# Kernel tuning notes

Measured on AMD Instinct MI355X. Metric: run time of the kernel, lower is better.

Reference implementation:

```python
import jax, jax.numpy as jnp
import numpy as np

SEQ, B, IN, H, L = 256, 512, 300, 512, 256
EPS = 1e-5


def setup_inputs() -> dict:
    key = jax.random.key(0)
    ks = jax.random.split(key, 10)
    s_ih = 1.0 / np.sqrt(H)
    return {
        "x": jax.random.normal(ks[0], (SEQ, B, IN), dtype=jnp.float32),
        "W_ih": jax.random.normal(ks[1], (4 * H, IN), dtype=jnp.float32) * s_ih,
        "W_hh": jax.random.normal(ks[2], (4 * H, H), dtype=jnp.float32) * s_ih,
        "b_ih": jax.random.normal(ks[3], (4 * H,), dtype=jnp.float32) * s_ih,
        "b_hh": jax.random.normal(ks[4], (4 * H,), dtype=jnp.float32) * s_ih,
        "bn1_gamma": jnp.ones((H,), dtype=jnp.float32),
        "bn1_beta": jnp.zeros((H,), dtype=jnp.float32),
        "W1": jax.random.normal(ks[5], (L, H), dtype=jnp.float32) / np.sqrt(H),
        "b1": jax.random.normal(ks[6], (L,), dtype=jnp.float32) * 0.01,
        "bn2_gamma": jnp.ones((L,), dtype=jnp.float32),
        "bn2_beta": jnp.zeros((L,), dtype=jnp.float32),
        "W2": jax.random.normal(ks[7], (1, L), dtype=jnp.float32) / np.sqrt(L),
        "b2": jax.random.normal(ks[8], (1,), dtype=jnp.float32) * 0.01,
    }


def _batchnorm(x, gamma, beta):
    # training-mode BatchNorm1d: batch statistics, biased variance
    mean = jnp.mean(x, axis=0)
    var = jnp.var(x, axis=0)
    return (x - mean) * jax.lax.rsqrt(var + EPS) * gamma + beta


def reference(x, W_ih, W_hh, b_ih, b_hh, bn1_gamma, bn1_beta, W1, b1,
              bn2_gamma, bn2_beta, W2, b2):
    # Pre-compute the input projection for all timesteps in one big GEMM:
    # [S, B, IN] @ [IN, 4H] -> [S, B, 4H]
    x_proj = jnp.einsum('sbi,gi->sbg', x, W_ih) + b_ih + b_hh

    def step(carry, xt):
        h, c = carry
        gates = xt + h @ W_hh.T  # [B, 4H]
        i, f, g, o = jnp.split(gates, 4, axis=-1)
        i = jax.nn.sigmoid(i)
        f = jax.nn.sigmoid(f)
        g = jnp.tanh(g)
        o = jax.nn.sigmoid(o)
        c = f * c + i * g
        h = o * jnp.tanh(c)
        return (h, c), None

    h0 = jnp.zeros((x.shape[1], H), dtype=x.dtype)
    c0 = jnp.zeros((x.shape[1], H), dtype=x.dtype)
    (h, _c), _ = jax.lax.scan(step, (h0, c0), x_proj)
    # dropout with training=False -> identity

    h = _batchnorm(h, bn1_gamma, bn1_beta)
    h = h @ W1.T + b1
    h = _batchnorm(h, bn2_gamma, bn2_beta)
    h = jax.nn.relu(h)
    out = h @ W2.T + b2            # [B, 1]
    out = 4.0 * jax.nn.sigmoid(out)
    return out.squeeze(-1)         # [B]
```

## Files before the change

### kernel.cpp

```cpp
#include <hip/hip_runtime.h>
#include <math.h>

constexpr int SEQ   = 256;
constexpr int BATCH = 512;
constexpr int INDIM = 300;
constexpr int KIH   = 320;
constexpr int HDIM  = 512;
constexpr int LDIM  = 256;
constexpr int G4    = 4 * HDIM;

typedef _Float16 f16x8 __attribute__((ext_vector_type(8)));
typedef _Float16 f16x4 __attribute__((ext_vector_type(4)));
typedef float    f32x4 __attribute__((ext_vector_type(4)));


__global__ __launch_bounds__(256) void prep_weights_kernel(
    const float* __restrict__ Wih, const float* __restrict__ Whh,
    const float* __restrict__ bih, const float* __restrict__ bhh,
    _Float16* __restrict__ slab, float* __restrict__ bsum)
{
    const int by = blockIdx.x >> 6;
    const int rl = blockIdx.x & 63;
    const int g  = rl >> 4, r = rl & 15;
    const int grow = g * HDIM + by * 16 + r;
    const int tid = threadIdx.x;
    if (tid < 208) {
        const int col0 = tid * 4;
        f16x4 v;
        #pragma unroll
        for (int e = 0; e < 4; ++e) {
            const int col = col0 + e;
            float f;
            if (col < KIH) f = (col < INDIM) ? Wih[(size_t)grow * INDIM + col] : 0.f;
            else           f = Whh[(size_t)grow * HDIM + (col - KIH)];
            v[e] = (_Float16)f;
        }
        *(f16x4*)(slab + ((size_t)(by * 64 + rl)) * 832 + col0) = v;
    } else if (tid == 208) {
        bsum[grow] = bih[grow] + bhh[grow];
    }
}

__global__ __launch_bounds__(256) void prep_x_kernel(
    const float* __restrict__ x, _Float16* __restrict__ xall)
{
    const int rowl = threadIdx.x >> 6;
    const int s    = threadIdx.x & 63;
    const int row  = blockIdx.x * 4 + rowl;
    if (s >= 40) return;
    const int k0 = s * 8;
    const float* xr = x + (size_t)row * INDIM;
    f16x8 v;
    #pragma unroll
    for (int e = 0; e < 8; ++e)
        v[e] = (k0 + e < INDIM) ? (_Float16)xr[k0 + e] : (_Float16)0.f;
    *(f16x8*)(xall + (size_t)row * KIH + k0) = v;
}

__global__ __launch_bounds__(256, 1) void lstm_persist(
    const _Float16* __restrict__ xall,
    const _Float16* __restrict__ slab,
    _Float16* __restrict__ hb,
    float* __restrict__ h32,
    const float* __restrict__ bsum,
    int* __restrict__ cnt)
{
    __shared__ _Float16 ring[2][64][88];
    __shared__ float    Gb[4][64][18];

    const int tid  = threadIdx.x;
    const int wid  = tid >> 6;
    const int lane = tid & 63;
    const int bx   = blockIdx.x & 7;
    const int by   = blockIdx.x >> 3;
    const int b0   = bx * 64;
    const int hc0  = by * 16;
    const int gh   = wid >> 1;
    const int bh   = wid & 1;
    const int l15  = lane & 15;
    const int q4   = lane >> 4;

    f16x8 wreg[13][2][2];
    {
        const _Float16* sb = slab + (size_t)by * 64 * 832;
        #pragma unroll
        for (int chv = 0; chv < 13; ++chv)
            #pragma unroll
            for (int kl = 0; kl < 2; ++kl)
                #pragma unroll
                for (int mt = 0; mt < 2; ++mt) {
                    const int rrow = gh * 32 + mt * 16 + l15;
                    const int kk   = chv * 64 + kl * 32 + q4 * 8;
                    wreg[chv][kl][mt] = *(const f16x8*)(sb + (size_t)rrow * 832 + kk);
                }
    }

    int srow[2], suu[2], woff[2];
    #pragma unroll
    for (int ii = 0; ii < 2; ++ii) {
        const int lin = ((wid * 2 + ii) << 10) + (lane << 4);
        srow[ii] = lin >> 7;
        suu[ii]  = (lin >> 4) & 7;
        woff[ii] = srow[ii] * 176 + suu[ii] * 16;
    }
    const int roffA = (bh * 32 + l15) * 176 + q4 * 16;
    const int roffB = roffA + 16 * 176;

    const int bl  = tid >> 2;
    const int j0l = (tid & 3) << 2;
    const int bg  = b0 + bl;
    const int jg  = hc0 + j0l;
    const f32x4 bi  = *(const f32x4*)&bsum[0 * HDIM + jg];
    const f32x4 bf  = *(const f32x4*)&bsum[1 * HDIM + jg];
    const f32x4 bgi = *(const f32x4*)&bsum[2 * HDIM + jg];
    const f32x4 bo  = *(const f32x4*)&bsum[3 * HDIM + jg];
    f32x4 cv = {0.f, 0.f, 0.f, 0.f};

    f16x8 rb[4][2];

#define BARX() do { asm volatile("" ::: "memory");                           \
                    __builtin_amdgcn_s_barrier();                            \
                    asm volatile("" ::: "memory"); } while (0)

#define LOADC(J, P) do {                                                     \
    _Pragma("unroll")                                                        \
    for (int ii = 0; ii < 2; ++ii) {                                         \
        if ((J) < 5) {                                                       \
            rb[((P)+(J)) & 3][ii] = *(const f16x8*)(xrow0 +                  \
                (size_t)srow[ii] * KIH + (((J) * 8 + suu[ii]) << 3));        \
        } else if ((J) < 13) {                                               \
            const unsigned long long* _p = (const unsigned long long*)       \
                (hrow0 + (size_t)srow[ii] * HDIM +                           \
                 ((((J) - 5) * 8 + suu[ii]) << 3));                          \
            union { unsigned long long u[2]; f16x8 v; } _t;                  \
            _t.u[0] = __hip_atomic_load(_p,     __ATOMIC_RELAXED,            \
                                        __HIP_MEMORY_SCOPE_AGENT);          \
            _t.u[1] = __hip_atomic_load(_p + 1, __ATOMIC_RELAXED,           \
                                        __HIP_MEMORY_SCOPE_AGENT);          \
            rb[((P)+(J)) & 3][ii] = _t.v;                                    \
        } else {                                                             \
            rb[((P)+(J)) & 3][ii] = *(const f16x8*)(xrow1 +                  \
                (size_t)srow[ii] * KIH + ((((J) - 13) * 8 + suu[ii]) << 3)); \
        }                                                                    \
    }                                                                        \
} while (0)

#define ITER(I, P, TT) do {                                                  \
    if ((I) == 1 && (TT) > 0) {                                              \
        const int* _fp = cnt + bx * 32 + (lane & 31);                        \
        int _wd = 0;                                                         \
        for (;;) {                                                           \
            const int _f = __hip_atomic_load(_fp, __ATOMIC_RELAXED,          \
                                             __HIP_MEMORY_SCOPE_AGENT);     \
            if (__all(_f >= (TT))) break;                                    \
            if (++_wd > (1 << 20)) break;                                    \
            __builtin_amdgcn_s_sleep(1);                                     \
        }                                                                    \
    }                                                                        \
    LOADC((I) + 4, P);                                                       \
    {                                                                        \
        char* _w = (char*)&ring[((P)+(I)+1) & 1][0][0];                      \
        _Pragma("unroll")                                                    \
        for (int ii = 0; ii < 2; ++ii)                                       \
            *(f16x8*)(_w + woff[ii]) = rb[((P)+(I)+1) & 3][ii];              \
    }                                                                        \
    {                                                                        \
        const char* _c = (const char*)&ring[((P)+(I)) & 1][0][0];            \
        _Pragma("unroll")                                                    \
        for (int kl = 0; kl < 2; ++kl) {                                     \
            const f16x8 b0f = *(const f16x8*)(_c + roffA + kl * 64);         \
            const f16x8 b1f = *(const f16x8*)(_c + roffB + kl * 64);         \
            acc00 = __builtin_amdgcn_mfma_f32_16x16x32_f16(wreg[I][kl][0], b0f, acc00, 0, 0, 0); \
            acc01 = __builtin_amdgcn_mfma_f32_16x16x32_f16(wreg[I][kl][0], b1f, acc01, 0, 0, 0); \
            acc10 = __builtin_amdgcn_mfma_f32_16x16x32_f16(wreg[I][kl][1], b0f, acc10, 0, 0, 0); \
            acc11 = __builtin_amdgcn_mfma_f32_16x16x32_f16(wreg[I][kl][1], b1f, acc11, 0, 0, 0); \
        }                                                                    \
    }                                                                        \
    asm volatile("s_waitcnt lgkmcnt(0)" ::: "memory");                       \
    BARX();                                                                  \
} while (0)

#define STEP(TT, P) do {                                                     \
    const _Float16* xrow0 = xall + ((size_t)(TT) * BATCH + b0) * KIH;        \
    const _Float16* xrow1 = xrow0 + (size_t)BATCH * KIH;                     \
    const _Float16* hrow0 = hb + (size_t)((P) & 1) * BATCH * HDIM            \
                               + (size_t)b0 * HDIM;                          \
    f32x4 acc00 = {0,0,0,0}, acc01 = {0,0,0,0},                              \
          acc10 = {0,0,0,0}, acc11 = {0,0,0,0};                              \
    ITER(0,P,TT); ITER(1,P,TT); ITER(2,P,TT); ITER(3,P,TT); ITER(4,P,TT);    \
    ITER(5,P,TT); ITER(6,P,TT); ITER(7,P,TT); ITER(8,P,TT); ITER(9,P,TT);    \
    ITER(10,P,TT); ITER(11,P,TT); ITER(12,P,TT);                             \
    {                                   \
        const int rbq = q4 * 4;                                              \
        _Pragma("unroll")                                                    \
        for (int q = 0; q < 4; ++q) {                                        \
            Gb[gh*2+0][bh*32 +      l15][rbq+q] = acc00[q];                  \
            Gb[gh*2+0][bh*32 + 16 + l15][rbq+q] = acc01[q];                  \
            Gb[gh*2+1][bh*32 +      l15][rbq+q] = acc10[q];                  \
            Gb[gh*2+1][bh*32 + 16 + l15][rbq+q] = acc11[q];                  \
        }                                                                    \
    }                                                                        \
    asm volatile("s_waitcnt lgkmcnt(0)" ::: "memory");                       \
    BARX();                                                                  \
    {                                 \
        f32x4 hv;                                                            \
        _Pragma("unroll")                                                    \
        for (int q = 0; q < 4; ++q) {                                        \
            float vi = Gb[0][bl][j0l+q] + bi[q];                             \
            float vf = Gb[1][bl][j0l+q] + bf[q];                             \
            float vg = Gb[2][bl][j0l+q] + bgi[q];                            \
            float vo = Gb[3][bl][j0l+q] + bo[q];                             \
            vi = 1.f / (1.f + __expf(-vi));                                  \
            vf = 1.f / (1.f + __expf(-vf));                                  \
            vg = 1.f - 2.f / (__expf(2.f * vg) + 1.f);   \
            vo = 1.f / (1.f + __expf(-vo));                                  \
            const float cc = vf * cv[q] + vi * vg;                           \
            cv[q] = cc;                                                      \
            hv[q] = vo * (1.f - 2.f / (__expf(2.f * cc) + 1.f));             \
        }                                                                    \
        union { unsigned long long u; f16x4 v; } hu;                         \
        hu.v[0]=(_Float16)hv[0]; hu.v[1]=(_Float16)hv[1];                    \
        hu.v[2]=(_Float16)hv[2]; hu.v[3]=(_Float16)hv[3];                    \
        _Float16* hbw = hb + (size_t)(((P)+1)&1) * BATCH * HDIM;             \
        __hip_atomic_store((unsigned long long*)(hbw + (size_t)bg*HDIM + jg),\
                           hu.u, __ATOMIC_RELAXED, __HIP_MEMORY_SCOPE_AGENT);\
        if ((TT) == SEQ-1) *(f32x4*)(h32 + (size_t)bg*HDIM + jg) = hv;       \
    }                                                                        \
    asm volatile("s_waitcnt vmcnt(0)" ::: "memory");                         \
    BARX();                                                                  \
    if (tid == 0)                                                            \
        __hip_atomic_store(&cnt[bx*32+by], (TT)+1, __ATOMIC_RELAXED,         \
                           __HIP_MEMORY_SCOPE_AGENT);                        \
} while (0)

    {
        const _Float16* xrow0 = xall + (size_t)b0 * KIH;
        const _Float16* xrow1 = xrow0 + (size_t)BATCH * KIH;
        const _Float16* hrow0 = hb;
        (void)xrow1; (void)hrow0;
        LOADC(0, 0); LOADC(1, 0); LOADC(2, 0); LOADC(3, 0);
        char* _w = (char*)&ring[0][0][0];
        #pragma unroll
        for (int ii = 0; ii < 2; ++ii)
            *(f16x8*)(_w + woff[ii]) = rb[0][ii];
        asm volatile("s_waitcnt lgkmcnt(0)" ::: "memory");
        BARX();
    }

    for (int tb = 0; tb < SEQ; tb += 4) {
        STEP(tb + 0, 0);
        STEP(tb + 1, 1);
        STEP(tb + 2, 2);
        STEP(tb + 3, 3);
    }
#undef BARX
#undef LOADC
#undef ITER
#undef STEP
}

__global__ __launch_bounds__(256) void prep_kernel(
    const float* __restrict__ Wih, const float* __restrict__ Whh,
    const float* __restrict__ bih, const float* __restrict__ bhh,
    _Float16* __restrict__ Wihc, _Float16* __restrict__ Whhc,
    float* __restrict__ bsum)
{
    const int g = blockIdx.x;
    for (int col = threadIdx.x; col < KIH; col += 256)
        Wihc[(size_t)g * KIH + col] =
            (col < INDIM) ? (_Float16)Wih[(size_t)g * INDIM + col] : (_Float16)0.f;
    for (int col = threadIdx.x; col < HDIM; col += 256)
        Whhc[(size_t)g * HDIM + col] = (_Float16)Whh[(size_t)g * HDIM + col];
    if (threadIdx.x == 0) bsum[g] = bih[g] + bhh[g];
}

__global__ __launch_bounds__(256) void fused_step_kernel(
    const float* __restrict__ xt, const _Float16* __restrict__ Wihc,
    const _Float16* __restrict__ Whhc, const float* __restrict__ bsum,
    float* __restrict__ c, float* __restrict__ h)
{
    __shared__ _Float16 As[32][72];
    __shared__ _Float16 Bs[128][72];
    __shared__ float    Gb[4][32][36];

    const int tid = threadIdx.x;
    const int b0  = blockIdx.x * 32;
    const int hc0 = blockIdx.y * 32;
    const int wid  = tid >> 6;
    const int lane = tid & 63;

    f32x4 acc[2][2] = {};
    const int arow = tid >> 3;
    const int ac8  = (tid & 7) * 8;
    const int brr  = tid >> 1;
    const int bseg = (tid & 1) * 32;

    for (int phase = 0; phase < 2; ++phase) {
        const float* Asrc = phase ? h : xt;
        const _Float16* Bsrc = phase ? Whhc : Wihc;
        const int Kpad = phase ? HDIM : KIH;
        const int Kval = phase ? HDIM : INDIM;
        const int astr = phase ? HDIM : INDIM;

        for (int k0 = 0; k0 < Kpad; k0 += 64) {
            const int gk = k0 + ac8;
            const float* pa = Asrc + (size_t)(b0 + arow) * astr + gk;
            float4 u = {0.f,0.f,0.f,0.f}, v = {0.f,0.f,0.f,0.f};
            if (gk + 3 < Kval)  u = *(const float4*)pa;
            if (gk + 7 < Kval)  v = *(const float4*)(pa + 4);
            f16x8 a8;
            a8[0]=(_Float16)u.x; a8[1]=(_Float16)u.y; a8[2]=(_Float16)u.z; a8[3]=(_Float16)u.w;
            a8[4]=(_Float16)v.x; a8[5]=(_Float16)v.y; a8[6]=(_Float16)v.z; a8[7]=(_Float16)v.w;
            const int grow = (brr >> 5) * HDIM + hc0 + (brr & 31);
            const _Float16* pb = Bsrc + (size_t)grow * Kpad + k0 + bseg;
            f16x8 w0 = *(const f16x8*)(pb + 0);
            f16x8 w1 = *(const f16x8*)(pb + 8);
            f16x8 w2 = *(const f16x8*)(pb + 16);
            f16x8 w3 = *(const f16x8*)(pb + 24);
            __syncthreads();
            *(f16x8*)&As[arow][ac8] = a8;
            *(f16x8*)&Bs[brr][bseg + 0]  = w0;
            *(f16x8*)&Bs[brr][bseg + 8]  = w1;
            *(f16x8*)&Bs[brr][bseg + 16] = w2;
            *(f16x8*)&Bs[brr][bseg + 24] = w3;
            __syncthreads();
            const int lr = lane & 15;
            const int lk = (lane >> 4) * 8;
            #pragma unroll
            for (int kf = 0; kf < 2; ++kf) {
                const int kl = kf * 32 + lk;
                f16x8 a0 = *(const f16x8*)&As[lr][kl];
                f16x8 a1 = *(const f16x8*)&As[16 + lr][kl];
                f16x8 bb0 = *(const f16x8*)&Bs[wid * 32 + lr][kl];
                f16x8 bb1 = *(const f16x8*)&Bs[wid * 32 + 16 + lr][kl];
                acc[0][0] = __builtin_amdgcn_mfma_f32_16x16x32_f16(a0, bb0, acc[0][0], 0, 0, 0);
                acc[0][1] = __builtin_amdgcn_mfma_f32_16x16x32_f16(a0, bb1, acc[0][1], 0, 0, 0);
                acc[1][0] = __builtin_amdgcn_mfma_f32_16x16x32_f16(a1, bb0, acc[1][0], 0, 0, 0);
                acc[1][1] = __builtin_amdgcn_mfma_f32_16x16x32_f16(a1, bb1, acc[1][1], 0, 0, 0);
            }
        }
    }
    __syncthreads();
    {
        const int cn = lane & 15;
        const int rbq = (lane >> 4) * 4;
        #pragma unroll
        for (int mi = 0; mi < 2; ++mi)
            #pragma unroll
            for (int ni = 0; ni < 2; ++ni)
                #pragma unroll
                for (int r = 0; r < 4; ++r)
                    Gb[wid][mi * 16 + rbq + r][ni * 16 + cn] = acc[mi][ni][r];
    }
    __syncthreads();
    {
        const int bl  = tid >> 3;
        const int jl0 = (tid & 7) * 4;
        const int gb  = b0 + bl;
        const int gj  = hc0 + jl0;
        const f32x4 ig = *(const f32x4*)&Gb[0][bl][jl0];
        const f32x4 fg = *(const f32x4*)&Gb[1][bl][jl0];
        const f32x4 gg = *(const f32x4*)&Gb[2][bl][jl0];
        const f32x4 og = *(const f32x4*)&Gb[3][bl][jl0];
        const f32x4 bi = *(const f32x4*)&bsum[0 * HDIM + gj];
        const f32x4 bf = *(const f32x4*)&bsum[1 * HDIM + gj];
        const f32x4 bg = *(const f32x4*)&bsum[2 * HDIM + gj];
        const f32x4 bo = *(const f32x4*)&bsum[3 * HDIM + gj];
        float* cp = c + (size_t)gb * HDIM + gj;
        float* hp = h + (size_t)gb * HDIM + gj;
        f32x4 cvv = *(const f32x4*)cp;
        f32x4 hv;
        #pragma unroll
        for (int q = 0; q < 4; ++q) {
            const float iv = 1.f / (1.f + __expf(-(ig[q] + bi[q])));
            const float fv = 1.f / (1.f + __expf(-(fg[q] + bf[q])));
            const float gv = tanhf(gg[q] + bg[q]);
            const float ov = 1.f / (1.f + __expf(-(og[q] + bo[q])));
            const float cc = fv * cvv[q] + iv * gv;
            cvv[q] = cc;
            hv[q] = ov * tanhf(cc);
        }
        *(f32x4*)cp = cvv;
        *(f32x4*)hp = hv;
    }
}

__global__ __launch_bounds__(256) void bn_stats_kernel(
    const float* __restrict__ X, int nfeat,
    const float* __restrict__ gamma, const float* __restrict__ beta,
    float* __restrict__ s, float* __restrict__ t)
{
    const int f = blockIdx.x * 256 + threadIdx.x;
    if (f >= nfeat) return;
    float sum = 0.f, sq = 0.f;
    for (int b = 0; b < BATCH; ++b) {
        const float v = X[(size_t)b * nfeat + f];
        sum += v; sq += v * v;
    }
    const float mean = sum * (1.f / BATCH);
    const float var  = sq * (1.f / BATCH) - mean * mean;
    const float rstd = rsqrtf(var + 1e-5f);
    const float sc   = gamma[f] * rstd;
    s[f] = sc;
    t[f] = beta[f] - mean * sc;
}

__global__ __launch_bounds__(256) void fc1_kernel(
    const float* __restrict__ h, const float* __restrict__ s1,
    const float* __restrict__ t1, const float* __restrict__ W1,
    const float* __restrict__ b1, float* __restrict__ out1)
{
    const int b = blockIdx.x;
    const int l = threadIdx.x;
    const float* hbp = h  + (size_t)b * HDIM;
    const float* wl  = W1 + (size_t)l * HDIM;
    float acc = 0.f;
    for (int k = 0; k < HDIM; ++k)
        acc += (hbp[k] * s1[k] + t1[k]) * wl[k];
    out1[(size_t)b * LDIM + l] = acc + b1[l];
}

__global__ __launch_bounds__(256) void final_kernel(
    const float* __restrict__ out1, const float* __restrict__ s2,
    const float* __restrict__ t2, const float* __restrict__ W2,
    const float* __restrict__ b2, float* __restrict__ out)
{
    const int b = blockIdx.x;
    float v = out1[(size_t)b * LDIM + threadIdx.x];
    v = v * s2[threadIdx.x] + t2[threadIdx.x];
    v = fmaxf(v, 0.f);
    v *= W2[threadIdx.x];
    #pragma unroll
    for (int off = 32; off > 0; off >>= 1) v += __shfl_down(v, off);
    __shared__ float red[4];
    if ((threadIdx.x & 63) == 0) red[threadIdx.x >> 6] = v;
    __syncthreads();
    if (threadIdx.x == 0) {
        const float ssum = red[0] + red[1] + red[2] + red[3] + b2[0];
        out[b] = 4.f / (1.f + expf(-ssum));
    }
}

extern "C" void kernel_launch(void* const* d_in, const int* in_sizes, int n_in,
                              void* d_out, int out_size, void* d_ws, size_t ws_size,
                              hipStream_t stream) {
    const float* x   = (const float*)d_in[0];
    const float* Wih = (const float*)d_in[1];
    const float* Whh = (const float*)d_in[2];
    const float* bih = (const float*)d_in[3];
    const float* bhh = (const float*)d_in[4];
    const float* g1  = (const float*)d_in[5];
    const float* be1 = (const float*)d_in[6];
    const float* W1  = (const float*)d_in[7];
    const float* b1  = (const float*)d_in[8];
    const float* g2  = (const float*)d_in[9];
    const float* be2 = (const float*)d_in[10];
    const float* W2  = (const float*)d_in[11];
    const float* b2  = (const float*)d_in[12];
    float* out = (float*)d_out;

    const size_t SZ_XALL = (size_t)SEQ * BATCH * KIH * 2;
    const size_t SZ_SLAB = (size_t)32 * 64 * 832 * 2;
    const size_t SZ_HB   = (size_t)2 * BATCH * HDIM * 2;
    const size_t SZ_H32  = (size_t)BATCH * HDIM * 4;
    const size_t SZ_BSUM = (size_t)G4 * 4;
    const size_t SZ_CNT  = (size_t)SEQ * 8 * 4;
    const size_t SZ_ST   = (size_t)(HDIM * 2 + LDIM * 2) * 4;
    const size_t SZ_OUT1 = (size_t)BATCH * LDIM * 4;
    const size_t NEED = SZ_XALL + SZ_SLAB + SZ_HB + SZ_H32 + SZ_BSUM +
                        SZ_CNT + SZ_ST + SZ_OUT1;

    if (ws_size >= NEED) {
        char* p = (char*)d_ws;
        _Float16* xall = (_Float16*)p;           p += SZ_XALL;
        _Float16* slab = (_Float16*)p;           p += SZ_SLAB;
        _Float16* hbuf = (_Float16*)p;           p += SZ_HB;
        float* h32     = (float*)p;              p += SZ_H32;
        float* bsum    = (float*)p;              p += SZ_BSUM;
        int*   cnt     = (int*)p;                p += SZ_CNT;
        float* s1 = (float*)p;                   p += HDIM * 4;
        float* t1 = (float*)p;                   p += HDIM * 4;
        float* s2 = (float*)p;                   p += LDIM * 4;
        float* t2 = (float*)p;                   p += LDIM * 4;
        float* out1 = (float*)p;

        hipMemsetAsync(hbuf, 0, SZ_HB, stream);
        hipMemsetAsync(cnt, 0, SZ_CNT, stream);
        prep_weights_kernel<<<2048, 256, 0, stream>>>(Wih, Whh, bih, bhh, slab, bsum);
        prep_x_kernel<<<SEQ * 128, 256, 0, stream>>>(x, xall);

        lstm_persist<<<dim3(256), dim3(256), 0, stream>>>(
            xall, slab, hbuf, h32, bsum, cnt);

        bn_stats_kernel<<<2, 256, 0, stream>>>(h32, HDIM, g1, be1, s1, t1);
        fc1_kernel<<<BATCH, 256, 0, stream>>>(h32, s1, t1, W1, b1, out1);
        bn_stats_kernel<<<1, 256, 0, stream>>>(out1, LDIM, g2, be2, s2, t2);
        final_kernel<<<BATCH, 256, 0, stream>>>(out1, s2, t2, W2, b2, out);
    } else {
        float* ws   = (float*)d_ws;
        float* h    = ws;
        float* c    = h + BATCH * HDIM;
        float* bsum = c + BATCH * HDIM;
        float* s1   = bsum + G4;
        float* t1   = s1 + HDIM;
        float* s2   = t1 + HDIM;
        float* t2   = s2 + LDIM;
        float* out1 = t2 + LDIM;
        _Float16* Wihc = (_Float16*)(out1 + (size_t)BATCH * LDIM);
        _Float16* Whhc = Wihc + (size_t)G4 * KIH;

        hipMemsetAsync(h, 0, (size_t)2 * BATCH * HDIM * sizeof(float), stream);
        prep_kernel<<<G4, 256, 0, stream>>>(Wih, Whh, bih, bhh, Wihc, Whhc, bsum);
        const dim3 sgrid(BATCH / 32, HDIM / 32);
        for (int t = 0; t < SEQ; ++t) {
            fused_step_kernel<<<sgrid, 256, 0, stream>>>(
                x + (size_t)t * BATCH * INDIM, Wihc, Whhc, bsum, c, h);
        }
        bn_stats_kernel<<<2, 256, 0, stream>>>(h, HDIM, g1, be1, s1, t1);
        fc1_kernel<<<BATCH, 256, 0, stream>>>(h, s1, t1, W1, b1, out1);
        bn_stats_kernel<<<1, 256, 0, stream>>>(out1, LDIM, g2, be2, s2, t2);
        final_kernel<<<BATCH, 256, 0, stream>>>(out1, s2, t2, W2, b2, out);
    }
}
```

Measured before the change: 1.347 ms.

## Load MFMA B-operands directly from global memory, removing LDS staging ring

Replaces the cooperative global-to-LDS ring buffer (with a barrier per K-chunk) by having each wave load its own MFMA B fragments straight from global memory into registers, prefetched three chunks ahead. This removes the per-chunk LDS writes, LDS reads and workgroup barriers from the recurrent step's critical path. In exchange the two wave halves issue duplicate global loads of the same x/h data, the loads are less coalesced, and register pressure rises. The x workspace is padded by one timestep so that prefetches past the last step stay in bounds.

```diff
diff --git a/kernel.cpp b/kernel.cpp
--- a/kernel.cpp
+++ b/kernel.cpp
@@ -65,8 +65,7 @@
     const float* __restrict__ bsum,
     int* __restrict__ cnt)
 {
-    __shared__ _Float16 ring[2][64][88];
-    __shared__ float    Gb[4][64][18];
+    __shared__ float Gb[4][64][18];
 
     const int tid  = threadIdx.x;
     const int wid  = tid >> 6;
@@ -95,16 +94,8 @@
                 }
     }
 
-    int srow[2], suu[2], woff[2];
-    #pragma unroll
-    for (int ii = 0; ii < 2; ++ii) {
-        const int lin = ((wid * 2 + ii) << 10) + (lane << 4);
-        srow[ii] = lin >> 7;
-        suu[ii]  = (lin >> 4) & 7;
-        woff[ii] = srow[ii] * 176 + suu[ii] * 16;
-    }
-    const int roffA = (bh * 32 + l15) * 176 + q4 * 16;
-    const int roffB = roffA + 16 * 176;
+    const size_t xoffb = (size_t)(b0 + bh * 32 + l15) * KIH  + q4 * 8;
+    const size_t hoffb = (size_t)(b0 + bh * 32 + l15) * HDIM + q4 * 8;
 
     const int bl  = tid >> 2;
     const int j0l = (tid & 3) << 2;
@@ -116,7 +107,7 @@
     const f32x4 bo  = *(const f32x4*)&bsum[3 * HDIM + jg];
     f32x4 cv = {0.f, 0.f, 0.f, 0.f};
 
-    f16x8 rb[4][2];
+    f16x8 fr[4][2][2];
 
 #define BARX() do { asm volatile("" ::: "memory");                           \
                     __builtin_amdgcn_s_barrier();                            \
@@ -124,25 +115,26 @@
 
 #define LOADC(J, P) do {                                                     \
     _Pragma("unroll")                                                        \
-    for (int ii = 0; ii < 2; ++ii) {                                         \
-        if ((J) < 5) {                                                       \
-            rb[((P)+(J)) & 3][ii] = *(const f16x8*)(xrow0 +                  \
-                (size_t)srow[ii] * KIH + (((J) * 8 + suu[ii]) << 3));        \
-        } else if ((J) < 13) {                                               \
-            const unsigned long long* _p = (const unsigned long long*)       \
-                (hrow0 + (size_t)srow[ii] * HDIM +                           \
-                 ((((J) - 5) * 8 + suu[ii]) << 3));                          \
-            union { unsigned long long u[2]; f16x8 v; } _t;                  \
-            _t.u[0] = __hip_atomic_load(_p,     __ATOMIC_RELAXED,            \
-                                        __HIP_MEMORY_SCOPE_AGENT);          \
-            _t.u[1] = __hip_atomic_load(_p + 1, __ATOMIC_RELAXED,           \
-                                        __HIP_MEMORY_SCOPE_AGENT);          \
-            rb[((P)+(J)) & 3][ii] = _t.v;                                    \
-        } else {                                                             \
-            rb[((P)+(J)) & 3][ii] = *(const f16x8*)(xrow1 +                  \
-                (size_t)srow[ii] * KIH + ((((J) - 13) * 8 + suu[ii]) << 3)); \
+    for (int nt = 0; nt < 2; ++nt)                                           \
+        _Pragma("unroll")                                                    \
+        for (int kl = 0; kl < 2; ++kl) {                                     \
+            if ((J) < 5) {                                                   \
+                fr[((P)+(J)) & 3][nt][kl] = *(const f16x8*)(xbase0 +         \
+                    (size_t)nt * (16 * KIH) + (J) * 64 + kl * 32);           \
+            } else if ((J) < 13) {                                           \
+                const unsigned long long* _p = (const unsigned long long*)   \
+                    (hbase + (size_t)nt * (16 * HDIM) + ((J)-5)*64 + kl*32); \
+                union { unsigned long long u[2]; f16x8 v; } _t;              \
+                _t.u[0] = __hip_atomic_load(_p,     __ATOMIC_RELAXED,        \
+                                            __HIP_MEMORY_SCOPE_AGENT);      \
+                _t.u[1] = __hip_atomic_load(_p + 1, __ATOMIC_RELAXED,       \
+                                            __HIP_MEMORY_SCOPE_AGENT);      \
+                fr[((P)+(J)) & 3][nt][kl] = _t.v;                            \
+            } else {                                                         \
+                fr[((P)+(J)) & 3][nt][kl] = *(const f16x8*)(xbase1 +         \
+                    (size_t)nt * (16 * KIH) + ((J)-13)*64 + kl*32);          \
+            }                                                                \
         }                                                                    \
-    }                                                                        \
 } while (0)
 
 #define ITER(I, P, TT) do {                                                  \
@@ -157,34 +149,20 @@
             __builtin_amdgcn_s_sleep(1);                                     \
         }                                                                    \
     }                                                                        \
-    LOADC((I) + 4, P);                                                       \
-    {                                                                        \
-        char* _w = (char*)&ring[((P)+(I)+1) & 1][0][0];                      \
-        _Pragma("unroll")                                                    \
-        for (int ii = 0; ii < 2; ++ii)                                       \
-            *(f16x8*)(_w + woff[ii]) = rb[((P)+(I)+1) & 3][ii];              \
+    if ((I) + 3 <= 15) LOADC((I) + 3, P);                                    \
+    _Pragma("unroll")                                                        \
+    for (int kl = 0; kl < 2; ++kl) {                                         \
+        acc00 = __builtin_amdgcn_mfma_f32_16x16x32_f16(wreg[I][kl][0], fr[((P)+(I)) & 3][0][kl], acc00, 0, 0, 0); \
+        acc01 = __builtin_amdgcn_mfma_f32_16x16x32_f16(wreg[I][kl][0], fr[((P)+(I)) & 3][1][kl], acc01, 0, 0, 0); \
+        acc10 = __builtin_amdgcn_mfma_f32_16x16x32_f16(wreg[I][kl][1], fr[((P)+(I)) & 3][0][kl], acc10, 0, 0, 0); \
+        acc11 = __builtin_amdgcn_mfma_f32_16x16x32_f16(wreg[I][kl][1], fr[((P)+(I)) & 3][1][kl], acc11, 0, 0, 0); \
     }                                                                        \
-    {                                                                        \
-        const char* _c = (const char*)&ring[((P)+(I)) & 1][0][0];            \
-        _Pragma("unroll")                                                    \
-        for (int kl = 0; kl < 2; ++kl) {                                     \
-            const f16x8 b0f = *(const f16x8*)(_c + roffA + kl * 64);         \
-            const f16x8 b1f = *(const f16x8*)(_c + roffB + kl * 64);         \
-            acc00 = __builtin_amdgcn_mfma_f32_16x16x32_f16(wreg[I][kl][0], b0f, acc00, 0, 0, 0); \
-            acc01 = __builtin_amdgcn_mfma_f32_16x16x32_f16(wreg[I][kl][0], b1f, acc01, 0, 0, 0); \
-            acc10 = __builtin_amdgcn_mfma_f32_16x16x32_f16(wreg[I][kl][1], b0f, acc10, 0, 0, 0); \
-            acc11 = __builtin_amdgcn_mfma_f32_16x16x32_f16(wreg[I][kl][1], b1f, acc11, 0, 0, 0); \
-        }                                                                    \
-    }                                                                        \
-    asm volatile("s_waitcnt lgkmcnt(0)" ::: "memory");                       \
-    BARX();                                                                  \
 } while (0)
 
 #define STEP(TT, P) do {                                                     \
-    const _Float16* xrow0 = xall + ((size_t)(TT) * BATCH + b0) * KIH;        \
-    const _Float16* xrow1 = xrow0 + (size_t)BATCH * KIH;                     \
-    const _Float16* hrow0 = hb + (size_t)((P) & 1) * BATCH * HDIM            \
-                               + (size_t)b0 * HDIM;                          \
+    const _Float16* xbase0 = xall + (size_t)(TT) * BATCH * KIH + xoffb;      \
+    const _Float16* xbase1 = xbase0 + (size_t)BATCH * KIH;                   \
+    const _Float16* hbase  = hb + (size_t)((TT) & 1) * BATCH * HDIM + hoffb; \
     f32x4 acc00 = {0,0,0,0}, acc01 = {0,0,0,0},                              \
           acc10 = {0,0,0,0}, acc11 = {0,0,0,0};                              \
     ITER(0,P,TT); ITER(1,P,TT); ITER(2,P,TT); ITER(3,P,TT); ITER(4,P,TT);    \
@@ -221,7 +199,7 @@
         union { unsigned long long u; f16x4 v; } hu;                         \
         hu.v[0]=(_Float16)hv[0]; hu.v[1]=(_Float16)hv[1];                    \
         hu.v[2]=(_Float16)hv[2]; hu.v[3]=(_Float16)hv[3];                    \
-        _Float16* hbw = hb + (size_t)(((P)+1)&1) * BATCH * HDIM;             \
+        _Float16* hbw = hb + (size_t)(((TT)+1)&1) * BATCH * HDIM;            \
         __hip_atomic_store((unsigned long long*)(hbw + (size_t)bg*HDIM + jg),\
                            hu.u, __ATOMIC_RELAXED, __HIP_MEMORY_SCOPE_AGENT);\
         if ((TT) == SEQ-1) *(f32x4*)(h32 + (size_t)bg*HDIM + jg) = hv;       \
@@ -234,17 +212,10 @@
 } while (0)
 
     {
-        const _Float16* xrow0 = xall + (size_t)b0 * KIH;
-        const _Float16* xrow1 = xrow0 + (size_t)BATCH * KIH;
-        const _Float16* hrow0 = hb;
-        (void)xrow1; (void)hrow0;
-        LOADC(0, 0); LOADC(1, 0); LOADC(2, 0); LOADC(3, 0);
-        char* _w = (char*)&ring[0][0][0];
-        #pragma unroll
-        for (int ii = 0; ii < 2; ++ii)
-            *(f16x8*)(_w + woff[ii]) = rb[0][ii];
-        asm volatile("s_waitcnt lgkmcnt(0)" ::: "memory");
-        BARX();
+        const _Float16* xbase0 = xall + xoffb;
+        const _Float16* xbase1 = xbase0 + (size_t)BATCH * KIH;  (void)xbase1;
+        const _Float16* hbase  = hb + hoffb;                    (void)hbase;
+        LOADC(0, 0); LOADC(1, 0); LOADC(2, 0);
     }
 
     for (int tb = 0; tb < SEQ; tb += 4) {
@@ -459,7 +430,7 @@
     const float* b2  = (const float*)d_in[12];
     float* out = (float*)d_out;
 
-    const size_t SZ_XALL = (size_t)SEQ * BATCH * KIH * 2;
+    const size_t SZ_XALL = (size_t)(SEQ + 1) * BATCH * KIH * 2;
     const size_t SZ_SLAB = (size_t)32 * 64 * 832 * 2;
     const size_t SZ_HB   = (size_t)2 * BATCH * HDIM * 2;
     const size_t SZ_H32  = (size_t)BATCH * HDIM * 4;
```

New measurement: 2.949 ms. 2.19x slower.
